# Optimization experiments

Hardware: AMD Instinct MI355X
Metric: run time of the kernel (lower is better)

The kernel has to match this reference:

```python
import jax, jax.numpy as jnp
import numpy as np

B, DIM, HID = 16384, 1024, 2048
HALF = DIM // 2
# alternating checkerboard mask: even indices are 'masked' (conditioning) dims
_MASK = np.arange(DIM) % 2 == 0
MASK_IDX = np.nonzero(_MASK)[0]      # dims fed to the MLP (static)
NEG_IDX = np.nonzero(~_MASK)[0]      # dims transformed by the affine coupling (static)


def setup_inputs() -> dict:
    key = jax.random.key(0)
    ks = jax.random.split(key, 8)
    s = 0.02  # small init so exp(s) stays well-behaved
    return {
        "z": jax.random.normal(ks[0], (B, DIM), jnp.float32),
        "log_det": jnp.zeros((B,), jnp.float32),
        "W1": jax.random.normal(ks[1], (HID, HALF), jnp.float32) * s,
        "b1": jax.random.normal(ks[2], (HID,), jnp.float32) * s,
        "W2": jax.random.normal(ks[3], (HID, HID), jnp.float32) * s,
        "b2": jax.random.normal(ks[4], (HID,), jnp.float32) * s,
        "W3": jax.random.normal(ks[5], (DIM, HID), jnp.float32) * s,
        "b3": jax.random.normal(ks[6], (DIM,), jnp.float32) * s,
    }


def reference(z, log_det, W1, b1, W2, b2, W3, b3):
    # gather conditioning dims (static column indices -> jit-friendly)
    zm = z[:, MASK_IDX]                                    # [B, HALF]
    # 3-layer MLP with exact (erf) GELU, matching torch nn.GELU default
    h = jax.nn.gelu(zm @ W1.T + b1, approximate=False)     # [B, HID]
    h = jax.nn.gelu(h @ W2.T + b2, approximate=False)      # [B, HID]
    s_t = h @ W3.T + b3                                    # [B, DIM]
    s, t = s_t[:, :HALF], s_t[:, HALF:]                    # each [B, HALF]
    # affine coupling on the complementary dims, scatter back (forward, inverse=False)
    z_out = z.at[:, NEG_IDX].set(z[:, NEG_IDX] * jnp.exp(s) + t)
    log_det_out = log_det + jnp.sum(s, axis=1)
    return z_out, log_det_out
```

## Files before the change

kernel.cpp:

```cpp
#include <hip/hip_runtime.h>
#include <hip/hip_bf16.h>
#include <cstdint>

typedef __bf16 bf16x8 __attribute__((ext_vector_type(8)));
typedef float  f32x4  __attribute__((ext_vector_type(4)));

struct alignas(4) us2 { unsigned short x, y; };
struct alignas(8) us4 { unsigned short x, y, z, w; };

__device__ __forceinline__ unsigned short f2bf(float f) {
    union { float f; unsigned u; } a; a.f = f;
    unsigned r = a.u + 0x7fffu + ((a.u >> 16) & 1u);
    return (unsigned short)(r >> 16);
}

__device__ __forceinline__ void gl_lds16(const void* g, void* s) {
    __builtin_amdgcn_global_load_lds(
        (const __attribute__((address_space(1))) void*)g,
        (__attribute__((address_space(3))) void*)s, 16, 0, 0);
}

#define SCHEDB()  __builtin_amdgcn_sched_barrier(0)
#define SBAR()    do { SCHEDB(); __builtin_amdgcn_s_barrier(); SCHEDB(); } while (0)
#define WAITLG(N) do { asm volatile("s_waitcnt lgkmcnt(" #N ")" ::: "memory"); SCHEDB(); } while (0)
#define WAITVM(N) do { asm volatile("s_waitcnt vmcnt(" #N ")" ::: "memory"); SCHEDB(); } while (0)

template<int EPI, int K, int N>
__global__ __launch_bounds__(512, 2)
void gemm256(const unsigned short* __restrict__ A,
             const unsigned short* __restrict__ W,
             const float* __restrict__ bias,
             unsigned short* __restrict__ outb,
             float* __restrict__ outf,
             const float* __restrict__ zin,
             float* __restrict__ ldout)
{
    extern __shared__ char smem[];
    constexpr int NH = K / 32;
    constexpr int GX = N / 256;

    const int tid  = threadIdx.x;
    const int lane = tid & 63;
    const int wv   = tid >> 6;
    const int wr   = wv >> 2, wc = wv & 3;

    const int bid = blockIdx.y * GX + blockIdx.x;
    const int nwg = GX * (int)gridDim.y;
    const int swz = (bid & 7) * (nwg >> 3) + (bid >> 3);
    const size_t row0 = (size_t)(swz / GX) * 256;
    const size_t col0 = (size_t)(swz % GX) * 256;

    const int cse = (((tid & 3) ^ ((tid >> 3) & 3)) << 3);
    const unsigned short* ag = A + (row0 + (tid >> 2)) * (size_t)K + cse;
    const unsigned short* bg = W + (col0 + (tid >> 2)) * (size_t)K + cse;

    auto stage = [&](int hh) {
        char* dA = smem + (hh & 3) * 16384 + tid * 16;
        char* dB = dA + 65536;
        const unsigned short* a = ag + (size_t)hh * 32;
        const unsigned short* b = bg + (size_t)hh * 32;
        gl_lds16(a,                     dA);
        gl_lds16(a + (size_t)128 * K,   dA + 8192);
        gl_lds16(b,                     dB);
        gl_lds16(b + (size_t)128 * K,   dB + 8192);
    };

    const int ln15 = lane & 15;
    const int xo   = (((lane >> 4) ^ ((ln15 >> 1) & 3)) << 4);
    const int arow = wr * 128 + ln15;
    const int brow = wc * 64 + ln15;

#define LD(base, row) (*(const bf16x8*)((base) + (size_t)(row) * 64 + xo))

    f32x4 acc[8][4] = {};

    stage(0); stage(1); stage(2);

    for (int h = 0; h < NH; ++h) {
        const char* cA = smem + (h & 3) * 16384;
        const char* cB = cA + 65536;

        if (h < NH - 2)       WAITVM(8);
        else if (h == NH - 2) WAITVM(4);
        else                  WAITVM(0);
        SBAR();

        bf16x8 aF[8], bF[4];
#pragma unroll
        for (int mf = 0; mf < 4; ++mf) aF[mf] = LD(cA, arow + mf * 16);
#pragma unroll
        for (int nf = 0; nf < 4; ++nf) bF[nf] = LD(cB, brow + nf * 16);
        SCHEDB();
#pragma unroll
        for (int mf = 4; mf < 8; ++mf) aF[mf] = LD(cA, arow + mf * 16);
        SCHEDB();
        if (h + 3 < NH) stage(h + 3);

        WAITLG(4);
        __builtin_amdgcn_s_setprio(1);
#pragma unroll
        for (int mf = 0; mf < 4; ++mf)
#pragma unroll
            for (int nf = 0; nf < 4; ++nf)
                acc[mf][nf] = __builtin_amdgcn_mfma_f32_16x16x32_bf16(
                    aF[mf], bF[nf], acc[mf][nf], 0, 0, 0);
        __builtin_amdgcn_s_setprio(0);

        WAITLG(0);
        __builtin_amdgcn_s_setprio(1);
#pragma unroll
        for (int mf = 4; mf < 8; ++mf)
#pragma unroll
            for (int nf = 0; nf < 4; ++nf)
                acc[mf][nf] = __builtin_amdgcn_mfma_f32_16x16x32_bf16(
                    aF[mf], bF[nf], acc[mf][nf], 0, 0, 0);
        __builtin_amdgcn_s_setprio(0);
    }
#undef LD

    const int lq = lane >> 4;
    float bv[4];
#pragma unroll
    for (int nf = 0; nf < 4; ++nf) bv[nf] = bias[col0 + wc * 64 + nf * 16 + ln15];

    if (EPI == 2) {
        const float2* zin2 = (const float2*)zin;
        float2*       out2 = (float2*)outf;
#pragma unroll
        for (int mi = 0; mi < 8; ++mi) {
#pragma unroll
            for (int r = 0; r < 4; ++r) {
                const size_t row = row0 + wr * 128 + mi * 16 + lq * 4 + r;
                float sv = 0.f;
#pragma unroll
                for (int p = 0; p < 2; ++p) {
                    float s = acc[mi][2 * p][r] + bv[2 * p];
                    float t = acc[mi][2 * p + 1][r] + bv[2 * p + 1];
                    const size_t j = (col0 >> 1) + wc * 32 + p * 16 + ln15;
                    float2 zv = zin2[row * 512 + j];
                    float2 o; o.x = zv.x; o.y = zv.y * __expf(s) + t;
                    out2[row * 512 + j] = o;
                    sv += s;
                }
                sv += __shfl_xor(sv, 1, 64);
                sv += __shfl_xor(sv, 2, 64);
                sv += __shfl_xor(sv, 4, 64);
                sv += __shfl_xor(sv, 8, 64);
                if (ln15 == 0) atomicAdd(&ldout[row], sv);
            }
        }
    } else {
#pragma unroll
        for (int mi = 0; mi < 8; ++mi) {
#pragma unroll
            for (int r = 0; r < 4; ++r) {
                const size_t row = row0 + wr * 128 + mi * 16 + lq * 4 + r;
#pragma unroll
                for (int nf = 0; nf < 4; ++nf) {
                    const size_t col = col0 + wc * 64 + nf * 16 + ln15;
                    float v = acc[mi][nf][r] + bv[nf];
                    if (EPI == 0) {
                        float g = 0.5f * v * (1.0f + erff(v * 0.70710678118654752f));
                        outb[row * N + col] = f2bf(g);
                    } else {
                        outf[row * N + col] = v;
                    }
                }
            }
        }
    }
}

__global__ void cvt_bf16(const float* __restrict__ in, unsigned short* __restrict__ out, int n4) {
    const int stride = gridDim.x * blockDim.x;
    for (int i = blockIdx.x * blockDim.x + threadIdx.x; i < n4; i += stride) {
        float4 v = ((const float4*)in)[i];
        us4 o{ f2bf(v.x), f2bf(v.y), f2bf(v.z), f2bf(v.w) };
        ((us4*)out)[i] = o;
    }
}

__global__ void cvt_w3i(const float* __restrict__ in, unsigned short* __restrict__ out, int n4) {
    const int stride = gridDim.x * blockDim.x;
    for (int i = blockIdx.x * blockDim.x + threadIdx.x; i < n4; i += stride) {
        int row = i >> 9;
        int c4  = i & 511;
        int q = row >> 5, u = row & 31;
        int srcrow = (u < 16) ? (q * 16 + u) : (512 + q * 16 + u - 16);
        float4 v = ((const float4*)in)[(size_t)srcrow * 512 + c4];
        us4 o{ f2bf(v.x), f2bf(v.y), f2bf(v.z), f2bf(v.w) };
        ((us4*)out)[i] = o;
    }
}

__global__ void pack_even(const float* __restrict__ z, unsigned short* __restrict__ zm, int n4) {
    const int stride = gridDim.x * blockDim.x;
    for (int i = blockIdx.x * blockDim.x + threadIdx.x; i < n4; i += stride) {
        float4 v = ((const float4*)z)[i];
        us2 o{ f2bf(v.x), f2bf(v.z) };
        ((us2*)zm)[i] = o;
    }
}

__global__ void prep3(const float* __restrict__ b3, float* __restrict__ b3i,
                      const float* __restrict__ ld, float* __restrict__ ldout, int nrow) {
    const int stride = gridDim.x * blockDim.x;
    int i = blockIdx.x * blockDim.x + threadIdx.x;
    if (i < 1024) {
        int q = i >> 5, u = i & 31;
        b3i[i] = b3[(u < 16) ? (q * 16 + u) : (512 + q * 16 + u - 16)];
    }
    for (int r = i; r < nrow; r += stride) ldout[r] = ld[r];
}

extern "C" void kernel_launch(void* const* d_in, const int* in_sizes, int n_in,
                              void* d_out, int out_size, void* d_ws, size_t ws_size,
                              hipStream_t stream)
{
    const float* z  = (const float*)d_in[0];
    const float* ld = (const float*)d_in[1];
    const float* W1 = (const float*)d_in[2];
    const float* b1 = (const float*)d_in[3];
    const float* W2 = (const float*)d_in[4];
    const float* b2 = (const float*)d_in[5];
    const float* W3 = (const float*)d_in[6];
    const float* b3 = (const float*)d_in[7];

    float* out   = (float*)d_out;
    float* zout  = out;
    float* ldout = out + (size_t)16384 * 1024;

    char* w = (char*)d_ws;
    unsigned short* zm  = (unsigned short*)w; w += (size_t)16384 * 512 * 2;
    unsigned short* w1b = (unsigned short*)w; w += (size_t)2048 * 512 * 2;
    unsigned short* w2b = (unsigned short*)w; w += (size_t)2048 * 2048 * 2;
    unsigned short* w3i = (unsigned short*)w; w += (size_t)1024 * 2048 * 2;
    unsigned short* h1  = (unsigned short*)w; w += (size_t)16384 * 2048 * 2;
    unsigned short* h2  = (unsigned short*)w; w += (size_t)16384 * 2048 * 2;
    float*          b3i = (float*)w;          w += 1024 * 4;

    (void)hipFuncSetAttribute((const void*)&gemm256<0, 512,  2048>,
                              hipFuncAttributeMaxDynamicSharedMemorySize, 131072);
    (void)hipFuncSetAttribute((const void*)&gemm256<0, 2048, 2048>,
                              hipFuncAttributeMaxDynamicSharedMemorySize, 131072);
    (void)hipFuncSetAttribute((const void*)&gemm256<2, 2048, 1024>,
                              hipFuncAttributeMaxDynamicSharedMemorySize, 131072);

    cvt_bf16 <<<512,  256, 0, stream>>>(W1, w1b, 2048 * 512 / 4);
    cvt_bf16 <<<2048, 256, 0, stream>>>(W2, w2b, 2048 * 2048 / 4);
    cvt_w3i  <<<1024, 256, 0, stream>>>(W3, w3i, 1024 * 2048 / 4);
    pack_even<<<2048, 256, 0, stream>>>(z, zm, 16384 * 1024 / 4);
    prep3    <<<64,   256, 0, stream>>>(b3, b3i, ld, ldout, 16384);

    gemm256<0, 512,  2048><<<dim3(8, 64), 512, 131072, stream>>>(zm, w1b, b1, h1, nullptr, nullptr, nullptr);
    gemm256<0, 2048, 2048><<<dim3(8, 64), 512, 131072, stream>>>(h1, w2b, b2, h2, nullptr, nullptr, nullptr);
    gemm256<2, 2048, 1024><<<dim3(4, 64), 512, 131072, stream>>>(h2, w3i, b3i, nullptr, zout, z, ldout);
}
```

Before: 332.2 us.

## Prefetch next K-step LDS fragments during MFMAs and fuse prep kernels

The GEMM main loop now loads the first half of the A and B fragments for the next K-slice from LDS while the second half of the current MFMAs runs. This software-pipelines LDS reads against MFMA work, and the vmem wait moves to an earlier stage. The five small conversion and prep kernels are merged into one grid-stride kernel to cut launch overhead. The cost is more VGPRs for the double-buffered fragments, which may lower occupancy or cause spills, plus branchy index dispatch in the prep kernel.

```diff
diff --git a/kernel.cpp b/kernel.cpp
--- a/kernel.cpp
+++ b/kernel.cpp
@@ -73,29 +73,28 @@
 #define LD(base, row) (*(const bf16x8*)((base) + (size_t)(row) * 64 + xo))
 
     f32x4 acc[8][4] = {};
+    bf16x8 pA[4], pB[4], nA[4], nB[4], aH[4];
 
     stage(0); stage(1); stage(2);
+    WAITVM(8);
+    SBAR();
+#pragma unroll
+    for (int mf = 0; mf < 4; ++mf) pA[mf] = LD(smem, arow + mf * 16);
+#pragma unroll
+    for (int nf = 0; nf < 4; ++nf) pB[nf] = LD(smem + 65536, brow + nf * 16);
 
     for (int h = 0; h < NH; ++h) {
-        const char* cA = smem + (h & 3) * 16384;
-        const char* cB = cA + 65536;
-
-        if (h < NH - 2)       WAITVM(8);
-        else if (h == NH - 2) WAITVM(4);
-        else                  WAITVM(0);
+        const char* cA  = smem + (h & 3) * 16384;
+        const char* cB  = cA + 65536;
+        const char* cAn = smem + ((h + 1) & 3) * 16384;
+        const char* cBn = cAn + 65536;
+
+        if (h <= NH - 3) WAITVM(4);
+        else             WAITVM(0);
         SBAR();
 
-        bf16x8 aF[8], bF[4];
-#pragma unroll
-        for (int mf = 0; mf < 4; ++mf) aF[mf] = LD(cA, arow + mf * 16);
-#pragma unroll
-        for (int nf = 0; nf < 4; ++nf) bF[nf] = LD(cB, brow + nf * 16);
-        SCHEDB();
-#pragma unroll
-        for (int mf = 4; mf < 8; ++mf) aF[mf] = LD(cA, arow + mf * 16);
-        SCHEDB();
-        if (h + 3 < NH) stage(h + 3);
-
+#pragma unroll
+        for (int mf = 0; mf < 4; ++mf) aH[mf] = LD(cA, arow + 64 + mf * 16);
         WAITLG(4);
         __builtin_amdgcn_s_setprio(1);
 #pragma unroll
@@ -103,18 +102,31 @@
 #pragma unroll
             for (int nf = 0; nf < 4; ++nf)
                 acc[mf][nf] = __builtin_amdgcn_mfma_f32_16x16x32_bf16(
-                    aF[mf], bF[nf], acc[mf][nf], 0, 0, 0);
+                    pA[mf], pB[nf], acc[mf][nf], 0, 0, 0);
         __builtin_amdgcn_s_setprio(0);
 
-        WAITLG(0);
+        if (h + 1 < NH) {
+#pragma unroll
+            for (int mf = 0; mf < 4; ++mf) nA[mf] = LD(cAn, arow + mf * 16);
+#pragma unroll
+            for (int nf = 0; nf < 4; ++nf) nB[nf] = LD(cBn, brow + nf * 16);
+            SCHEDB();
+        }
+        if (h + 3 < NH) stage(h + 3);
+
+        if (h + 1 < NH) WAITLG(8);
+        else            WAITLG(0);
         __builtin_amdgcn_s_setprio(1);
 #pragma unroll
-        for (int mf = 4; mf < 8; ++mf)
+        for (int mf = 0; mf < 4; ++mf)
 #pragma unroll
             for (int nf = 0; nf < 4; ++nf)
-                acc[mf][nf] = __builtin_amdgcn_mfma_f32_16x16x32_bf16(
-                    aF[mf], bF[nf], acc[mf][nf], 0, 0, 0);
+                acc[mf + 4][nf] = __builtin_amdgcn_mfma_f32_16x16x32_bf16(
+                    aH[mf], pB[nf], acc[mf + 4][nf], 0, 0, 0);
         __builtin_amdgcn_s_setprio(0);
+
+#pragma unroll
+        for (int i = 0; i < 4; ++i) { pA[i] = nA[i]; pB[i] = nB[i]; }
     }
 #undef LD
 
@@ -171,46 +183,58 @@
     }
 }
 
-__global__ void cvt_bf16(const float* __restrict__ in, unsigned short* __restrict__ out, int n4) {
+__global__ void prep_all(const float* __restrict__ W1, const float* __restrict__ W2,
+                         const float* __restrict__ W3, const float* __restrict__ b3,
+                         const float* __restrict__ z,  const float* __restrict__ ld,
+                         unsigned short* __restrict__ w1b, unsigned short* __restrict__ w2b,
+                         unsigned short* __restrict__ w3i, float* __restrict__ b3i,
+                         unsigned short* __restrict__ zm,  float* __restrict__ ldout)
+{
+    constexpr int N1 = 2048 * 512 / 4;
+    constexpr int N2 = 2048 * 2048 / 4;
+    constexpr int N3 = 1024 * 2048 / 4;
+    constexpr int N4 = 16384 * 1024 / 4;
+    constexpr int N5 = 1024;
+    constexpr int N6 = 16384;
+    constexpr int TOT = N1 + N2 + N3 + N4 + N5 + N6;
     const int stride = gridDim.x * blockDim.x;
-    for (int i = blockIdx.x * blockDim.x + threadIdx.x; i < n4; i += stride) {
-        float4 v = ((const float4*)in)[i];
-        us4 o{ f2bf(v.x), f2bf(v.y), f2bf(v.z), f2bf(v.w) };
-        ((us4*)out)[i] = o;
+    for (int i = blockIdx.x * blockDim.x + threadIdx.x; i < TOT; i += stride) {
+        int j = i;
+        if (j < N1) {
+            float4 v = ((const float4*)W1)[j];
+            ((us4*)w1b)[j] = us4{ f2bf(v.x), f2bf(v.y), f2bf(v.z), f2bf(v.w) };
+            continue;
+        }
+        j -= N1;
+        if (j < N2) {
+            float4 v = ((const float4*)W2)[j];
+            ((us4*)w2b)[j] = us4{ f2bf(v.x), f2bf(v.y), f2bf(v.z), f2bf(v.w) };
+            continue;
+        }
+        j -= N2;
+        if (j < N3) {
+            int row = j >> 9, c4 = j & 511;
+            int q = row >> 5, u = row & 31;
+            int srcrow = (u < 16) ? (q * 16 + u) : (512 + q * 16 + u - 16);
+            float4 v = ((const float4*)W3)[(size_t)srcrow * 512 + c4];
+            ((us4*)w3i)[j] = us4{ f2bf(v.x), f2bf(v.y), f2bf(v.z), f2bf(v.w) };
+            continue;
+        }
+        j -= N3;
+        if (j < N4) {
+            float4 v = ((const float4*)z)[j];
+            ((us2*)zm)[j] = us2{ f2bf(v.x), f2bf(v.z) };
+            continue;
+        }
+        j -= N4;
+        if (j < N5) {
+            int q = j >> 5, u = j & 31;
+            b3i[j] = b3[(u < 16) ? (q * 16 + u) : (512 + q * 16 + u - 16)];
+            continue;
+        }
+        j -= N5;
+        ldout[j] = ld[j];
     }
-}
-
-__global__ void cvt_w3i(const float* __restrict__ in, unsigned short* __restrict__ out, int n4) {
-    const int stride = gridDim.x * blockDim.x;
-    for (int i = blockIdx.x * blockDim.x + threadIdx.x; i < n4; i += stride) {
-        int row = i >> 9;
-        int c4  = i & 511;
-        int q = row >> 5, u = row & 31;
-        int srcrow = (u < 16) ? (q * 16 + u) : (512 + q * 16 + u - 16);
-        float4 v = ((const float4*)in)[(size_t)srcrow * 512 + c4];
-        us4 o{ f2bf(v.x), f2bf(v.y), f2bf(v.z), f2bf(v.w) };
-        ((us4*)out)[i] = o;
-    }
-}
-
-__global__ void pack_even(const float* __restrict__ z, unsigned short* __restrict__ zm, int n4) {
-    const int stride = gridDim.x * blockDim.x;
-    for (int i = blockIdx.x * blockDim.x + threadIdx.x; i < n4; i += stride) {
-        float4 v = ((const float4*)z)[i];
-        us2 o{ f2bf(v.x), f2bf(v.z) };
-        ((us2*)zm)[i] = o;
-    }
-}
-
-__global__ void prep3(const float* __restrict__ b3, float* __restrict__ b3i,
-                      const float* __restrict__ ld, float* __restrict__ ldout, int nrow) {
-    const int stride = gridDim.x * blockDim.x;
-    int i = blockIdx.x * blockDim.x + threadIdx.x;
-    if (i < 1024) {
-        int q = i >> 5, u = i & 31;
-        b3i[i] = b3[(u < 16) ? (q * 16 + u) : (512 + q * 16 + u - 16)];
-    }
-    for (int r = i; r < nrow; r += stride) ldout[r] = ld[r];
 }
 
 extern "C" void kernel_launch(void* const* d_in, const int* in_sizes, int n_in,
@@ -246,11 +270,8 @@
     (void)hipFuncSetAttribute((const void*)&gemm256<2, 2048, 1024>,
                               hipFuncAttributeMaxDynamicSharedMemorySize, 131072);
 
-    cvt_bf16 <<<512,  256, 0, stream>>>(W1, w1b, 2048 * 512 / 4);
-    cvt_bf16 <<<2048, 256, 0, stream>>>(W2, w2b, 2048 * 2048 / 4);
-    cvt_w3i  <<<1024, 256, 0, stream>>>(W3, w3i, 1024 * 2048 / 4);
-    pack_even<<<2048, 256, 0, stream>>>(z, zm, 16384 * 1024 / 4);
-    prep3    <<<64,   256, 0, stream>>>(b3, b3i, ld, ldout, 16384);
+    prep_all<<<2048, 256, 0, stream>>>(W1, W2, W3, b3, z, ld,
+                                       w1b, w2b, w3i, b3i, zm, ldout);
 
     gemm256<0, 512,  2048><<<dim3(8, 64), 512, 131072, stream>>>(zm, w1b, b1, h1, nullptr, nullptr, nullptr);
     gemm256<0, 2048, 2048><<<dim3(8, 64), 512, 131072, stream>>>(h1, w2b, b2, h2, nullptr, nullptr, nullptr);
```

Result: faster. 317.1 us (-4.6%).
